# Optimization experiments

Hardware: AMD Instinct MI355X
Metric: run time of the kernel (lower is better)

The kernel has to match this reference:

```python
import jax, jax.numpy as jnp
import numpy as np

# ---- static config (mirrors forward() defaults of NeuSRenderer) ----
NV = 32
FOV = 60.0            # degrees
BIN_SIZE = 0.015
NUM_BINS = 128
RAY_U, RAY_V = 64, 8  # coarse ray grid -> 512 rays per view
NUM_PDF_RAYS = 64
STEP_COARSE = 256     # base step samples per ray (multiple of NUM_BINS)
NUM_PDF_STEPS = 32
RADIUS = 1.0
COS_ANNEAL = 0.0
HID = 64


def sdf_fn(pts, W1, b1, w2, b2):
    # pts [..., 3] -> sdf [...]
    h = jax.nn.softplus(pts @ W1 + b1)
    return h @ w2 + b2[0]


def sdf_grad(pts, W1, b1, w2):
    # analytic gradient of sdf_fn w.r.t. pts (softplus' = sigmoid)
    s = jax.nn.sigmoid(pts @ W1 + b1)          # [..., HID]
    return jnp.einsum('...h,dh->...d', s * w2, W1)


def inside_hemisphere(pts, radius):
    return (jnp.linalg.norm(pts, axis=-1) < radius) & (pts[..., 2] > 0)


def sample_rays(key, Rt, fov, usize, vsize, pdf=None, npdf=None):
    nv = Rt.shape[0]
    ns = usize * vsize
    uu, vv = jnp.meshgrid(jnp.arange(usize, dtype=jnp.float32),
                          jnp.arange(vsize, dtype=jnp.float32), indexing='ij')
    u, v = uu.ravel(), vv.ravel()
    k1, k2, k3, k4, k5 = jax.random.split(key, 5)
    ru = (u[None] + jax.random.uniform(k1, (nv, ns))) / usize
    rv = (v[None] + jax.random.uniform(k2, (nv, ns))) / vsize
    uv_idx = jnp.broadcast_to(jnp.arange(ns), (nv, ns))
    if pdf is not None:
        # Multinomial(counts) + repeat_interleave == npdf categorical draws
        idx = jax.random.categorical(k3, jnp.log(pdf + 1e-6), shape=(npdf, nv)).T  # [nv, npdf]
        cnts = jnp.zeros((nv, ns)).at[jnp.arange(nv)[:, None], idx].add(1.0)
        ru_p = (u[idx] + jax.random.uniform(k4, (nv, npdf))) / usize
        rv_p = (v[idx] + jax.random.uniform(k5, (nv, npdf))) / vsize
        w = 1.0 / ((cnts + 1.0) * ns)
        w = jnp.concatenate((w, jnp.take_along_axis(w, idx, axis=1)), axis=-1)
        ru = jnp.concatenate((ru, ru_p), axis=-1)
        rv = jnp.concatenate((rv, rv_p), axis=-1)
        uv_idx = jnp.concatenate((uv_idx, idx), axis=-1)
    else:
        w = jnp.ones_like(ru) / ns
    min_cos = np.float32(np.cos(fov * np.pi / 360.0))
    solid_angle = np.float32(2 * np.pi * (1 - min_cos))
    phi = ru * np.float32(2 * np.pi)
    cos_t = rv * (1 - min_cos) + min_cos
    sin_t = jnp.sqrt(jnp.clip(1 - cos_t ** 2, 0.0))
    d = jnp.stack((sin_t * jnp.cos(phi), sin_t * jnp.sin(phi), cos_t), axis=-1)
    o = Rt[..., -1]                                       # [nv, 3]
    d = jnp.einsum('vnj,vij->vni', d, Rt[..., :3])        # rotate to world
    w = w * cos_t * solid_angle
    sg = jax.lax.stop_gradient                            # torch.no_grad()
    return sg(o), sg(d), sg(w), uv_idx


def sample_steps(key, v, r, bin_size, nb, ns, pdf=None, npdf=None):
    k1, k2, k3 = jax.random.split(key, 3)
    edges1 = bin_size * jnp.arange(nb + 1, dtype=jnp.float32)
    edges = jnp.broadcast_to(edges1, (v, r, nb + 1))
    left = edges[..., :-1, None]                          # [v,r,nb,1]
    etas = jax.random.uniform(k1, (v, r, nb, ns // nb - 1)) * bin_size
    steps = jnp.concatenate((left, left + etas), axis=-1).reshape(v, r, ns)
    steps = jnp.concatenate((steps, edges[..., -1:]), axis=-1)  # [v,r,ns+1]
    if pdf is not None:
        bidx = jax.random.categorical(k2, jnp.log(pdf + 1e-6),
                                      shape=(npdf, v, r)).transpose(1, 2, 0)
        le = jnp.take_along_axis(edges, bidx, axis=-1)
        steps = jnp.concatenate((steps, le + jax.random.uniform(k3, le.shape) * bin_size), axis=-1)
    return jax.lax.stop_gradient(jnp.sort(steps, axis=-1))


def run_coarse(key, Rt, W1, b1, w2, b2):
    k1, k2 = jax.random.split(key)
    o, d, _, _ = sample_rays(k1, Rt, FOV, RAY_U, RAY_V)
    nv, nr = d.shape[:2]
    steps = sample_steps(k2, nv, nr, BIN_SIZE, NUM_BINS, STEP_COARSE)
    deltas = steps[..., 1:] - steps[..., :-1]
    pts = o[:, None, None, :] + steps[..., None] * d[:, :, None, :]   # [v,r,S+1,3]
    sdf = sdf_fn(pts, W1, b1, w2, b2)
    mid_pts = 0.5 * (pts[..., 1:, :] + pts[..., :-1, :])
    mid_sdf = 0.5 * (sdf[..., 1:] + sdf[..., :-1])
    cos = (sdf[..., 1:] - sdf[..., :-1]) / (deltas + 1e-6)
    prev_cos = jnp.concatenate((jnp.zeros_like(cos[..., :1]), cos[..., :-1]), axis=-1)
    cos = jnp.clip(jnp.minimum(prev_cos, cos), -1000.0, 0.0)
    dsdf = 0.5 * cos * deltas
    prev_T = jax.nn.sigmoid(64.0 * (mid_sdf - dsdf))
    next_T = jax.nn.sigmoid(64.0 * (mid_sdf + dsdf))
    alpha = (1 - next_T / (prev_T + 1e-6)) * inside_hemisphere(mid_pts, RADIUS)
    T = jnp.cumprod(jnp.concatenate((jnp.ones_like(alpha[..., :1]),
                                     (1 - alpha[..., :-1]) ** 2 + 1e-6), axis=-1), axis=-1)
    weights = (alpha * T).reshape(nv, nr, NUM_BINS, -1)
    step_pdf = weights.sum(-1)
    ray_pdf = step_pdf.sum(-1)
    sg = jax.lax.stop_gradient
    return sg(ray_pdf), sg(step_pdf)


def bin_scatter(vals, bidx, nb):
    # equivalent to einsum('vrpb,vrp->vrb', one_hot(bidx), vals), memory-light
    v, r, p = vals.shape
    return jnp.zeros((v, r, nb), vals.dtype).at[
        jnp.arange(v)[:, None, None], jnp.arange(r)[None, :, None], bidx].add(vals)


def run_fine(key, Rt, W1, b1, w2, b2, inv_s, rho, ray_pdf, step_pdf):
    k1, k2 = jax.random.split(key)
    o, d, w, uv_idx = sample_rays(k1, Rt, FOV, RAY_U, RAY_V, ray_pdf, NUM_PDF_RAYS)
    nv, nr = d.shape[:2]
    spdf = step_pdf[jnp.arange(nv)[:, None], uv_idx]                  # gather per ray
    steps_e = sample_steps(k2, nv, nr, BIN_SIZE, NUM_BINS, STEP_COARSE, spdf, NUM_PDF_STEPS)
    deltas = steps_e[..., 1:] - steps_e[..., :-1]
    steps = 0.5 * (steps_e[..., 1:] + steps_e[..., :-1])              # midpoints [v,r,P]
    pts = o[:, None, None, :] + steps[..., None] * d[:, :, None, :]
    ins = inside_hemisphere(pts, RADIUS)
    insf = ins.astype(pts.dtype)
    sdf = sdf_fn(pts, W1, b1, w2, b2) * insf                          # zeros outside (masked_scatter)
    normal = sdf_grad(pts, W1, b1, w2) * insf[..., None]
    cos = jnp.einsum('vrj,vrpj->vrp', d, normal)
    ac = -(jax.nn.relu(-cos * 0.5 + 0.5) * (1 - COS_ANNEAL) + jax.nn.relu(-cos) * COS_ANNEAL)
    dsdf = 0.5 * ac * deltas
    prev_T = jax.nn.sigmoid(inv_s * (sdf - dsdf))
    next_T = jax.nn.sigmoid(inv_s * (sdf + dsdf))
    alpha = (1 - next_T / (prev_T + 1e-6)) * insf
    T = jnp.cumprod(jnp.concatenate((jnp.ones_like(alpha[..., :1]),
                                     (1 - alpha[..., :-1]) ** 2), axis=-1), axis=-1)
    weights = alpha * T
    radiance = weights * (rho * (-ac / (steps ** 2 + 1e-6)))          # brdf_net = rho * x
    bidx = jnp.clip(jnp.floor(steps / BIN_SIZE).astype(jnp.int32), 0, NUM_BINS - 1)
    valid = ((steps > bidx * BIN_SIZE) & (steps < (bidx + 1) * BIN_SIZE)).astype(steps.dtype)
    bin_alpha = bin_scatter(alpha * valid, bidx, NUM_BINS)
    bin_weights = bin_scatter(weights * valid, bidx, NUM_BINS)
    opacity = bin_weights.sum(-1)
    rad_bins = bin_scatter(radiance * valid, bidx, NUM_BINS)
    hists = jnp.sum(rad_bins * w[..., None], axis=-2)                 # [nv, NUM_BINS]
    return hists, sdf, normal, alpha, T, weights, bin_alpha, bin_weights, opacity


def setup_inputs() -> dict:
    key = jax.random.key(0)
    ks = jax.random.split(key, 7)
    R, _ = jnp.linalg.qr(jax.random.normal(ks[0], (NV, 3, 3)))        # random rotations
    t = jax.random.normal(ks[1], (NV, 3)) * 0.1 + jnp.array([0.0, 0.0, 0.15])
    Rt = jnp.concatenate((R, t[..., None]), axis=-1).astype(jnp.float32)
    W1 = 0.5 * jax.random.normal(ks[2], (3, HID), dtype=jnp.float32)
    b1 = 0.1 * jax.random.normal(ks[3], (HID,), dtype=jnp.float32)
    w2 = 0.3 * jax.random.normal(ks[4], (HID,), dtype=jnp.float32)
    b2 = jnp.array([0.05], dtype=jnp.float32)
    inv_s = jnp.array([64.0], dtype=jnp.float32)
    rho = jnp.array([0.5], dtype=jnp.float32)
    return {"Rt": Rt, "W1": W1, "b1": b1, "w2": w2, "b2": b2, "inv_s": inv_s, "rho": rho}


def reference(Rt, W1, b1, w2, b2, inv_s, rho):
    key = jax.random.key(42)
    kc, kf = jax.random.split(key)
    ray_pdf, step_pdf = run_coarse(kc, Rt, W1, b1, w2, b2)
    outs = run_fine(kf, Rt, W1, b1, w2, b2, inv_s, rho, ray_pdf, step_pdf)
    return (*outs, ray_pdf.reshape(Rt.shape[0], RAY_U, RAY_V), step_pdf)
```

## Files before the change

kernel.cpp:

```cpp
#include <hip/hip_runtime.h>
#include <stdint.h>
#include <math.h>


#define NS    512
#define NB    128
#define NCS   257
#define NPS   32
#define NFS   289
#define NFM   288
#define HID   64

#define O_HISTS  0
#define O_SDF    4096
#define O_NORMAL 5312512
#define O_ALPHA  21237760
#define O_T      26546176
#define O_W      31854592
#define O_BA     37163008
#define O_BW     39522304
#define O_OP     41881600
#define O_RPDF   41900032
#define O_SPDF   41916416

#define DEC_RT   0
#define DEC_W1   384
#define DEC_B1   576
#define DEC_W2   640
#define DEC_B2   704
#define DEC_INVS 705
#define DEC_RHO  706
#define DEC_G    707

__host__ __device__ inline void tf2x32(uint32_t k0, uint32_t k1,
                                       uint32_t x0, uint32_t x1,
                                       uint32_t& o0, uint32_t& o1) {
  uint32_t ks2 = k0 ^ k1 ^ 0x1BD11BDAu;
  x0 += k0; x1 += k1;
#define TFR(r) { x0 += x1; x1 = (x1 << (r)) | (x1 >> (32 - (r))); x1 ^= x0; }
  TFR(13) TFR(15) TFR(26) TFR(6)
  x0 += k1;  x1 += ks2 + 1u;
  TFR(17) TFR(29) TFR(16) TFR(24)
  x0 += ks2; x1 += k0 + 2u;
  TFR(13) TFR(15) TFR(26) TFR(6)
  x0 += k0;  x1 += k1 + 3u;
  TFR(17) TFR(29) TFR(16) TFR(24)
  x0 += k1;  x1 += ks2 + 4u;
  TFR(13) TFR(15) TFR(26) TFR(6)
  x0 += ks2; x1 += k0 + 5u;
#undef TFR
  o0 = x0; o1 = x1;
}

__device__ inline uint32_t rbits(uint2 k, uint32_t i) {
  uint32_t a, b; tf2x32(k.x, k.y, 0u, i, a, b);
  return a ^ b;
}

__device__ inline float u01(uint32_t bits) {
  return __uint_as_float(0x3f800000u | (bits >> 9)) - 1.0f;
}
__device__ inline float gumbelf(uint32_t bits) {
  float f = u01(bits);
  float u = (f > 0.0f) ? f : 1.17549435082228751e-38f;
  return -logf(-logf(u));
}
__device__ inline float sigmoidf_(float x) {
  return __fdiv_rn(1.0f, __fadd_rn(1.0f, expf(-x)));
}
__device__ inline float softplusf_(float x) {
  return __fadd_rn(fmaxf(x, 0.0f), log1pf(expf(-fabsf(x))));
}
__device__ inline float frcp_(float x) { return __builtin_amdgcn_rcpf(x); }
__device__ inline float fsig_(float x) { return frcp_(1.0f + __expf(-x)); }
__device__ inline void argmax_reduce64(float& best, int& bi) {
  for (int off = 1; off < 64; off <<= 1) {
    float ob = __shfl_xor(best, off);
    int   oi = __shfl_xor(bi, off);
    if (ob > best || (ob == best && oi < bi)) { best = ob; bi = oi; }
  }
}

static void jax_split(const uint32_t k[2], int n, uint32_t out[][2]) {
  for (int j = 0; j < n; j++)
    tf2x32(k[0], k[1], 0u, (uint32_t)j, out[j][0], out[j][1]);
}
static inline uint2 mkk(const uint32_t k[2]) { return make_uint2(k[0], k[1]); }

__device__ inline float ld_as(const void* p, int i, int isbf) {
  if (isbf) {
    uint16_t h = ((const uint16_t*)p)[i];
    return __uint_as_float(((uint32_t)h) << 16);
  }
  return ((const float*)p)[i];
}

__global__ void k_decode(const void* Rt, const void* W1, const void* b1,
                         const void* w2, const void* b2, const void* invs,
                         const void* rho, float* dec) {
  __shared__ int sflag;
  if (threadIdx.x == 0) {
    float errF = 0.0f, errB = 0.0f;
    for (int v = 0; v < 8; v++)
      for (int row = 0; row < 3; row++) {
        float nF = 0.0f, nB = 0.0f;
        for (int j = 0; j < 3; j++) {
          float aF = ld_as(Rt, v * 12 + row * 4 + j, 0); nF += aF * aF;
          float aB = ld_as(Rt, v * 12 + row * 4 + j, 1); nB += aB * aB;
        }
        errF += fabsf(nF - 1.0f); errB += fabsf(nB - 1.0f);
      }
    int pickF = (errF == errF) && (!(errB == errB) || errF < errB);
    sflag = pickF ? 0 : 1;
  }
  __syncthreads();
  int f = sflag, t = threadIdx.x;
  for (int i = t; i < 384; i += 256) dec[DEC_RT + i] = ld_as(Rt, i, f);
  if (t < 192) dec[DEC_W1 + t] = ld_as(W1, t, f);
  if (t < 64)  dec[DEC_B1 + t] = ld_as(b1, t, f);
  if (t < 64)  dec[DEC_W2 + t] = ld_as(w2, t, f);
  if (t == 0) {
    dec[DEC_B2]   = ld_as(b2, 0, f);
    dec[DEC_INVS] = ld_as(invs, 0, f);
    dec[DEC_RHO]  = ld_as(rho, 0, f);
    float G = 0.0f;
    for (int j = 0; j < 64; j++) {
      float wx = ld_as(W1, j, f), wy = ld_as(W1, 64 + j, f), wz = ld_as(W1, 128 + j, f);
      G += fabsf(ld_as(w2, j, f)) * sqrtf(wx * wx + wy * wy + wz * wz);
    }
    dec[DEC_G] = G * 1.02f + 0.001f;
  }
}

__global__ void k_zero(int* __restrict__ cnts) {
  int i = blockIdx.x * 256 + threadIdx.x;
  if (i < 16384) cnts[i] = 0;
}

__global__ void __launch_bounds__(64) k_coarse(
    const float* __restrict__ dec,
    uint2 k_ru, uint2 k_rv, uint2 k_eta, float mc, float omc,
    float* __restrict__ c_step_pdf, float* __restrict__ c_ray_pdf,
    float* __restrict__ out) {
  int r = blockIdx.x, v = blockIdx.y, lane = threadIdx.x;
  __shared__ float4 sW4[64];
  __shared__ float  sw2[64];
  __shared__ float ss[NCS], sfa[NCS], sfe[NCS], salpha[256], sflagf[256];
  __shared__ int   slist[NCS], scls[256];
  if (lane < 64) {
    sW4[lane] = make_float4(dec[DEC_W1 + lane], dec[DEC_W1 + 64 + lane],
                            dec[DEC_W1 + 128 + lane], dec[DEC_B1 + lane]);
    sw2[lane] = dec[DEC_W2 + lane];
  }
  float b2 = dec[DEC_B2];
  float G  = dec[DEC_G];
  float Gm = fminf(1000.0f, G);
  float alpha_c = __fsub_rn(1.0f, __fdiv_rn(1.0f, __fadd_rn(1.0f, 1e-6f)));

  uint32_t li = (uint32_t)(v * NS + r);
  float un = (float)(r >> 3), vn = (float)(r & 7);
  float ru = __fdiv_rn(__fadd_rn(un, u01(rbits(k_ru, li))), 64.0f);
  float rv = __fdiv_rn(__fadd_rn(vn, u01(rbits(k_rv, li))), 8.0f);
  float phi = __fmul_rn(ru, (float)(2.0 * M_PI));
  float ct  = __fadd_rn(__fmul_rn(rv, omc), mc);
  float stq = sqrtf(fmaxf(__fsub_rn(1.0f, __fmul_rn(ct, ct)), 0.0f));
  float dc0 = __fmul_rn(stq, cosf(phi));
  float dc1 = __fmul_rn(stq, sinf(phi));
  const float* Rv = dec + DEC_RT + v * 12;
  float o0 = Rv[3], o1 = Rv[7], o2 = Rv[11];
  float d0 = dc0 * Rv[0] + dc1 * Rv[1] + ct * Rv[2];
  float d1 = dc0 * Rv[4] + dc1 * Rv[5] + ct * Rv[6];
  float d2 = dc0 * Rv[8] + dc1 * Rv[9] + ct * Rv[10];

  for (int p = lane; p < NCS; p += 64) {
    float sp;
    if (p == 256) sp = __fmul_rn(0.015f, 128.0f);
    else {
      int b = p >> 1;
      float eb = __fmul_rn(0.015f, (float)b);
      if (p & 1) {
        float u = u01(rbits(k_eta, li * 128u + (uint32_t)b));
        sp = __fadd_rn(eb, __fmul_rn(u, 0.015f));
      } else sp = eb;
    }
    ss[p] = sp;
  }
  __syncthreads();

  for (int p = lane; p < 256; p += 64) {
    float s0 = ss[p], s1 = ss[p + 1];
    float ax = __fadd_rn(o0, __fmul_rn(s0, d0)), bx = __fadd_rn(o0, __fmul_rn(s1, d0));
    float ay = __fadd_rn(o1, __fmul_rn(s0, d1)), by = __fadd_rn(o1, __fmul_rn(s1, d1));
    float az = __fadd_rn(o2, __fmul_rn(s0, d2)), bz = __fadd_rn(o2, __fmul_rn(s1, d2));
    float mx = __fmul_rn(0.5f, __fadd_rn(ax, bx));
    float my = __fmul_rn(0.5f, __fadd_rn(ay, by));
    float mz = __fmul_rn(0.5f, __fadd_rn(az, bz));
    float n2 = __fadd_rn(__fadd_rn(__fmul_rn(mx, mx), __fmul_rn(my, my)), __fmul_rn(mz, mz));
    bool ins = (sqrtf(n2) < 1.0f) && (mz > 0.0f);
    sflagf[p] = ins ? 1.0f : 0.0f;
  }
  __syncthreads();

  int ncnt = 0;
  for (int c = 0; c < 5; c++) {
    int p = c * 64 + lane;
    bool need = false;
    if (p < NCS) {
      bool f0 = (p >= 1) ? (sflagf[p - 1] != 0.0f) : false;
      bool f1 = (p < 256) ? (sflagf[p] != 0.0f) : false;
      bool f2 = (p + 1 < 256) ? (sflagf[p + 1] != 0.0f) : false;
      need = f0 || f1 || f2;
    }
    unsigned long long m = __ballot(need);
    int idx = ncnt + __popcll(m & ((1ull << lane) - 1ull));
    if (need) slist[idx] = p;
    ncnt += __popcll(m);
  }
  __syncthreads();

  for (int k = lane; k < ncnt; k += 64) {
    int p = slist[k];
    float sp = ss[p];
    float px = fmaf(sp, d0, o0);
    float py = fmaf(sp, d1, o1);
    float pz = fmaf(sp, d2, o2);
    float acc = 0.0f;
    for (int j = 0; j < HID; j++) {
      float4 q = sW4[j];
      float t = fmaf(px, q.x, fmaf(py, q.y, fmaf(pz, q.z, q.w)));
      float e = __expf(-fabsf(t));
      acc = fmaf(fmaxf(t, 0.0f) + __logf(1.0f + e), sw2[j], acc);
    }
    sfa[p] = acc + b2;
  }
  __syncthreads();

  for (int p = lane; p < 256; p += 64) {
    int cls = 0;
    if (sflagf[p] != 0.0f) {
      float delta = __fsub_rn(ss[p + 1], ss[p]);
      float Bd = 0.5f * delta * Gm * 1.01f + 1e-6f;
      float ma = 0.5f * (sfa[p] + sfa[p + 1]);
      float margin = Bd + 0.02f;
      if (ma - margin > 0.28f)       cls = 1;
      else if (ma + margin < -0.52f) cls = 2;
      else                            cls = 3;
    }
    scls[p] = cls;
  }
  __syncthreads();

  int ecnt = 0;
  for (int c = 0; c < 5; c++) {
    int p = c * 64 + lane;
    bool need = false;
    if (p < NCS) {
      bool f0 = (p >= 1) ? (scls[p - 1] == 3) : false;
      bool f1 = (p < 256) ? (scls[p] == 3) : false;
      bool f2 = (p + 1 < 256) ? (scls[p + 1] == 3) : false;
      need = f0 || f1 || f2;
    }
    unsigned long long m = __ballot(need);
    int idx = ecnt + __popcll(m & ((1ull << lane) - 1ull));
    if (need) slist[idx] = p;
    ecnt += __popcll(m);
  }
  __syncthreads();

  for (int k = lane; k < ecnt; k += 64) {
    int p = slist[k];
    float sp = ss[p];
    float px = __fadd_rn(o0, __fmul_rn(sp, d0));
    float py = __fadd_rn(o1, __fmul_rn(sp, d1));
    float pz = __fadd_rn(o2, __fmul_rn(sp, d2));
    float acc = 0.0f;
    for (int j = 0; j < HID; j++) {
      float4 q = sW4[j];
      float t = fmaf(px, q.x, fmaf(py, q.y, fmaf(pz, q.z, q.w)));
      acc = fmaf(softplusf_(t), sw2[j], acc);
    }
    sfe[p] = __fadd_rn(acc, b2);
  }
  __syncthreads();

  for (int p = lane; p < 256; p += 64) {
    int cls = scls[p];
    float a;
    if (cls == 0)      a = 0.0f;
    else if (cls == 1) a = alpha_c;
    else if (cls == 2) a = 1.0f;
    else {
      float s0 = ss[p], s1 = ss[p + 1];
      float f0 = sfe[p], f1 = sfe[p + 1];
      float delta = __fsub_rn(s1, s0);
      float mid_sdf = __fmul_rn(0.5f, __fadd_rn(f1, f0));
      float cosv = __fdiv_rn(__fsub_rn(f1, f0), __fadd_rn(delta, 1e-6f));
      float pcos = 0.0f;
      if (p > 0)
        pcos = __fdiv_rn(__fsub_rn(f0, sfe[p - 1]),
                         __fadd_rn(__fsub_rn(s0, ss[p - 1]), 1e-6f));
      float cc = fminf(fmaxf(fminf(pcos, cosv), -1000.0f), 0.0f);
      float dsdf = __fmul_rn(__fmul_rn(0.5f, cc), delta);
      float pT = sigmoidf_(__fmul_rn(64.0f, __fsub_rn(mid_sdf, dsdf)));
      float nT = sigmoidf_(__fmul_rn(64.0f, __fadd_rn(mid_sdf, dsdf)));
      a = __fmul_rn(__fsub_rn(1.0f, __fdiv_rn(nT, __fadd_rn(pT, 1e-6f))), 1.0f);
    }
    salpha[p] = a;
  }
  __syncthreads();

  if (lane == 0) {
    float T = 1.0f, rsum = 0.0f;
    int base = (v * NS + r) * NB;
    for (int b = 0; b < NB; b++) {
      float a0 = salpha[2 * b], a1 = salpha[2 * b + 1];
      float w0 = __fmul_rn(a0, T);
      float om = __fsub_rn(1.0f, a0);
      T = __fmul_rn(T, __fadd_rn(__fmul_rn(om, om), 1e-6f));
      float w1 = __fmul_rn(a1, T);
      om = __fsub_rn(1.0f, a1);
      T = __fmul_rn(T, __fadd_rn(__fmul_rn(om, om), 1e-6f));
      float spdf = __fadd_rn(w0, w1);
      c_step_pdf[base + b] = spdf;
      out[O_SPDF + base + b] = spdf;
      rsum = __fadd_rn(rsum, spdf);
    }
    c_ray_pdf[v * NS + r] = rsum;
    out[O_RPDF + v * NS + r] = rsum;
  }
}

__global__ void __launch_bounds__(64) k_raycat(
    const float* __restrict__ c_ray_pdf, uint2 kg,
    int* __restrict__ f_idx, int* __restrict__ cnts) {
  int p = blockIdx.x, v = blockIdx.y, lane = threadIdx.x;
  uint32_t rowbase = ((uint32_t)p * 32u + (uint32_t)v) * 512u;
  float best = -INFINITY; int bi = 0;
  for (int n = lane; n < 512; n += 64) {
    float lg = logf(__fadd_rn(c_ray_pdf[v * 512 + n], 1e-6f));
    float val = __fadd_rn(gumbelf(rbits(kg, rowbase + (uint32_t)n)), lg);
    if (val > best) { best = val; bi = n; }
  }
  argmax_reduce64(best, bi);
  if (lane == 0) {
    f_idx[v * 64 + p] = bi;
    atomicAdd(&cnts[v * 512 + bi], 1);
  }
}

__global__ void __launch_bounds__(64) k_stepcat(
    const float* __restrict__ c_step_pdf, const int* __restrict__ f_idx,
    uint2 kg, int* __restrict__ bidx) {
  int r = blockIdx.x, v = blockIdx.y, lane = threadIdx.x;
  int n = (r < 512) ? r : f_idx[v * 64 + (r - 512)];
  const float* pdfrow = c_step_pdf + (v * 512 + n) * 128;
  float lg0 = logf(__fadd_rn(pdfrow[lane], 1e-6f));
  float lg1 = logf(__fadd_rn(pdfrow[64 + lane], 1e-6f));
  for (int p = 0; p < 32; p++) {
    uint32_t base = (((uint32_t)p * 32u + (uint32_t)v) * 576u + (uint32_t)r) * 128u;
    float v0 = __fadd_rn(gumbelf(rbits(kg, base + (uint32_t)lane)), lg0);
    float v1 = __fadd_rn(gumbelf(rbits(kg, base + 64u + (uint32_t)lane)), lg1);
    float best = v0; int bi = lane;
    if (v1 > best) { best = v1; bi = 64 + lane; }
    argmax_reduce64(best, bi);
    if (lane == 0) bidx[(v * 576 + r) * 32 + p] = bi;
  }
}

__global__ void __launch_bounds__(64) k_fine(
    const float* __restrict__ dec, const int* __restrict__ f_idx,
    const int* __restrict__ cnts, const int* __restrict__ bidx,
    uint2 k_ru, uint2 k_rv, uint2 k_rup, uint2 k_rvp, uint2 k_eta, uint2 k_us,
    float mc, float omc, float sa,
    float* __restrict__ rad_rows, float* __restrict__ out) {
  int r = blockIdx.x, v = blockIdx.y, lane = threadIdx.x;
  __shared__ float4 sW4[64];
  __shared__ float  sw2[64];
  __shared__ float sb[NCS], pe[NPS], st[NFS];
  __shared__ float sal[NFM], sac[NFM], sT[NFM];
  __shared__ int   slist[NFM];
  __shared__ float bina[NB], binw[NB], binr[NB];
  if (lane < 64) {
    sW4[lane] = make_float4(dec[DEC_W1 + lane], dec[DEC_W1 + 64 + lane],
                            dec[DEC_W1 + 128 + lane], dec[DEC_B1 + lane]);
    sw2[lane] = dec[DEC_W2 + lane];
  }
  bina[lane] = 0.0f; binw[lane] = 0.0f; binr[lane] = 0.0f;
  bina[64 + lane] = 0.0f; binw[64 + lane] = 0.0f; binr[64 + lane] = 0.0f;
  float b2 = dec[DEC_B2], inv_s = dec[DEC_INVS], rho = dec[DEC_RHO];

  int n; float ruB, rvB;
  if (r < 512) {
    n = r;
    ruB = u01(rbits(k_ru, (uint32_t)(v * 512 + r)));
    rvB = u01(rbits(k_rv, (uint32_t)(v * 512 + r)));
  } else {
    int p = r - 512;
    n = f_idx[v * 64 + p];
    ruB = u01(rbits(k_rup, (uint32_t)(v * 64 + p)));
    rvB = u01(rbits(k_rvp, (uint32_t)(v * 64 + p)));
  }
  float un = (float)(n >> 3), vn = (float)(n & 7);
  float ru = __fdiv_rn(__fadd_rn(un, ruB), 64.0f);
  float rv = __fdiv_rn(__fadd_rn(vn, rvB), 8.0f);
  float phi = __fmul_rn(ru, (float)(2.0 * M_PI));
  float ct  = __fadd_rn(__fmul_rn(rv, omc), mc);
  float stq = sqrtf(fmaxf(__fsub_rn(1.0f, __fmul_rn(ct, ct)), 0.0f));
  float dc0 = __fmul_rn(stq, cosf(phi));
  float dc1 = __fmul_rn(stq, sinf(phi));
  const float* Rv = dec + DEC_RT + v * 12;
  float o0 = Rv[3], o1 = Rv[7], o2 = Rv[11];
  float d0 = dc0 * Rv[0] + dc1 * Rv[1] + ct * Rv[2];
  float d1 = dc0 * Rv[4] + dc1 * Rv[5] + ct * Rv[6];
  float d2 = dc0 * Rv[8] + dc1 * Rv[9] + ct * Rv[10];
  float wb = __fdiv_rn(1.0f, __fmul_rn(__fadd_rn((float)cnts[v * 512 + n], 1.0f), 512.0f));
  float wray = __fmul_rn(__fmul_rn(wb, ct), sa);

  uint32_t li = (uint32_t)(v * 576 + r);
  for (int p = lane; p < NCS; p += 64) {
    float sp;
    if (p == 256) sp = __fmul_rn(0.015f, 128.0f);
    else {
      int b = p >> 1;
      float eb = __fmul_rn(0.015f, (float)b);
      if (p & 1) {
        float u = u01(rbits(k_eta, li * 128u + (uint32_t)b));
        sp = __fadd_rn(eb, __fmul_rn(u, 0.015f));
      } else sp = eb;
    }
    sb[p] = sp;
  }
  if (lane < NPS) {
    int b = bidx[(v * 576 + r) * 32 + lane];
    float le = __fmul_rn(0.015f, (float)b);
    float u = u01(rbits(k_us, li * 32u + (uint32_t)lane));
    pe[lane] = __fadd_rn(le, __fmul_rn(u, 0.015f));
  }
  __syncthreads();

  for (int c = 0; c < 5; c++) {
    int p = c * 64 + lane;
    if (p < NCS) {
      float x = sb[p];
      int cntlt = 0;
      for (int j = 0; j < NPS; j++) cntlt += (pe[j] < x) ? 1 : 0;
      st[p + cntlt] = x;
    }
  }
  if (lane < NPS) {
    float x = pe[lane];
    int lo = 0, hi = NCS;
    while (lo < hi) { int m = (lo + hi) >> 1; if (sb[m] <= x) lo = m + 1; else hi = m; }
    int rk = 0;
    for (int j = 0; j < NPS; j++) {
      float y = pe[j];
      rk += (y < x || (y == x && j < lane)) ? 1 : 0;
    }
    st[lo + rk] = x;
  }
  __syncthreads();

  size_t obase = (size_t)(v * 576 + r) * NFM;
  int cnt = 0;
  for (int c = 0; c < 5; c++) {
    int p = c * 64 + lane;
    bool f = false;
    if (p < NFM) {
      float s0 = st[p], s1 = st[p + 1];
      float mid = __fmul_rn(0.5f, __fadd_rn(s1, s0));
      float px = __fadd_rn(o0, __fmul_rn(mid, d0));
      float py = __fadd_rn(o1, __fmul_rn(mid, d1));
      float pz = __fadd_rn(o2, __fmul_rn(mid, d2));
      float n2 = __fadd_rn(__fadd_rn(__fmul_rn(px, px), __fmul_rn(py, py)), __fmul_rn(pz, pz));
      f = (sqrtf(n2) < 1.0f) && (pz > 0.0f);
      sal[p] = 0.0f; sac[p] = 0.0f;
      if (!f) {
        out[O_SDF + obase + p] = 0.0f;
        out[O_ALPHA + obase + p] = 0.0f;
        size_t nb3 = (obase + p) * 3;
        out[O_NORMAL + nb3] = 0.0f;
        out[O_NORMAL + nb3 + 1] = 0.0f;
        out[O_NORMAL + nb3 + 2] = 0.0f;
      }
    }
    unsigned long long m = __ballot(f);
    int idx = cnt + __popcll(m & ((1ull << lane) - 1ull));
    if (f) slist[idx] = p;
    cnt += __popcll(m);
  }
  __syncthreads();

  for (int k = lane; k < cnt; k += 64) {
    int p = slist[k];
    float s0 = st[p], s1 = st[p + 1];
    float delta = s1 - s0;
    float mid = 0.5f * (s1 + s0);
    float px = fmaf(mid, d0, o0);
    float py = fmaf(mid, d1, o1);
    float pz = fmaf(mid, d2, o2);
    float acc = 0.0f, g0 = 0.0f, g1 = 0.0f, g2 = 0.0f;
    for (int j = 0; j < HID; j++) {
      float4 q = sW4[j];
      float t = fmaf(px, q.x, fmaf(py, q.y, fmaf(pz, q.z, q.w)));
      float e = __expf(-fabsf(t));
      float w2j = sw2[j];
      acc = fmaf(fmaxf(t, 0.0f) + __logf(1.0f + e), w2j, acc);
      float rr = frcp_(1.0f + e);
      float sg = (t >= 0.0f) ? rr : e * rr;
      float m = sg * w2j;
      g0 = fmaf(m, q.x, g0);
      g1 = fmaf(m, q.y, g1);
      g2 = fmaf(m, q.z, g2);
    }
    float sdf = acc + b2;
    float cosr = fmaf(d0, g0, fmaf(d1, g1, d2 * g2));
    float ac = -fmaxf(fmaf(-cosr, 0.5f, 0.5f), 0.0f);
    float dsdf = 0.5f * ac * delta;
    float pT = fsig_(inv_s * (sdf - dsdf));
    float nT = fsig_(inv_s * (sdf + dsdf));
    float alpha = 1.0f - nT * frcp_(pT + 1e-6f);
    sal[p] = alpha; sac[p] = ac;
    out[O_SDF + obase + p] = sdf;
    size_t nb3 = (obase + p) * 3;
    out[O_NORMAL + nb3]     = g0;
    out[O_NORMAL + nb3 + 1] = g1;
    out[O_NORMAL + nb3 + 2] = g2;
    out[O_ALPHA + obase + p] = alpha;
  }
  __syncthreads();

  {
    int q0 = lane * 5, q1 = q0 + 5 > NFM ? NFM : q0 + 5;
    float lp = 1.0f;
    for (int q = q0; q < q1; q++) { float om = 1.0f - sal[q]; lp *= om * om; }
    float x = lp;
    for (int d = 1; d < 64; d <<= 1) {
      float y = __shfl_up(x, d);
      if (lane >= d) x *= y;
    }
    float excl = __shfl_up(x, 1);
    if (lane == 0) excl = 1.0f;
    float T = excl;
    for (int q = q0; q < q1; q++) {
      sT[q] = T;
      float om = 1.0f - sal[q];
      T *= om * om;
    }
  }
  __syncthreads();

  for (int c = 0; c < 5; c++) {
    int p = c * 64 + lane;
    if (p < NFM) {
      float T = sT[p], a = sal[p];
      float wgt = a * T;
      out[O_T + obase + p] = T;
      out[O_W + obase + p] = wgt;
      float s0 = st[p], s1 = st[p + 1];
      float mid = __fmul_rn(0.5f, __fadd_rn(s1, s0));
      int bi = (int)floorf(__fdiv_rn(mid, 0.015f));
      bi = bi < 0 ? 0 : (bi > 127 ? 127 : bi);
      bool valid = (mid > __fmul_rn((float)bi, 0.015f)) &&
                   (mid < __fmul_rn((float)(bi + 1), 0.015f));
      if (valid) {
        atomicAdd(&bina[bi], a);
        atomicAdd(&binw[bi], wgt);
        float inner = (-sac[p]) * frcp_(fmaf(mid, mid, 1e-6f));
        atomicAdd(&binr[bi], wgt * rho * inner);
      }
    }
  }
  __syncthreads();

  size_t bb = (size_t)(v * 576 + r) * NB;
  for (int c = 0; c < 2; c++) {
    int b = c * 64 + lane;
    out[O_BA + bb + b] = bina[b];
    out[O_BW + bb + b] = binw[b];
    rad_rows[bb + b] = __fmul_rn(binr[b], wray);
  }
  float opv = binw[lane] + binw[64 + lane];
  for (int d = 32; d; d >>= 1) opv += __shfl_xor(opv, d);
  if (lane == 0) out[O_OP + (size_t)(v * 576 + r)] = opv;
}

__global__ void __launch_bounds__(256) k_final(
    const float* __restrict__ rad_rows, float* __restrict__ out) {
  int idx = blockIdx.x * 4 + (threadIdx.x >> 6);
  int lane = threadIdx.x & 63;
  if (idx < 4096) {
    int v = idx >> 7, b = idx & 127;
    const float* base = rad_rows + (size_t)v * 576 * 128 + b;
    float s = 0.0f;
    for (int k = 0; k < 9; k++)
      s += base[(size_t)(lane + 64 * k) * 128];
    for (int d = 32; d; d >>= 1) s += __shfl_xor(s, d);
    if (lane == 0) out[O_HISTS + idx] = s;
  }
}

extern "C" void kernel_launch(void* const* d_in, const int* in_sizes, int n_in,
                              void* d_out, int out_size, void* d_ws, size_t ws_size,
                              hipStream_t stream) {
  float* out = (float*)d_out;

  const size_t WS_NEED = 5081856u * 4u;
  if (n_in != 7) { hipMemsetAsync(d_out, 0x75, 4, stream); return; }
  static const int want[7] = {384, 192, 64, 64, 1, 1, 1};
  for (int i = 0; i < 7; i++)
    if (in_sizes[i] != want[i]) { hipMemsetAsync(d_out, 0x74, 4, stream); return; }
  if (ws_size < WS_NEED) { hipMemsetAsync(d_out, 0x77, 4, stream); return; }
  (void)out_size;

  uint32_t root[2] = {0u, 42u};
  uint32_t kcf[2][2]; jax_split(root, 2, kcf);
  uint32_t ck[2][2];  jax_split(kcf[0], 2, ck);
  uint32_t crk[5][2]; jax_split(ck[0], 5, crk);
  uint32_t csk[3][2]; jax_split(ck[1], 3, csk);
  uint32_t fk2[2][2]; jax_split(kcf[1], 2, fk2);
  uint32_t frk[5][2]; jax_split(fk2[0], 5, frk);
  uint32_t fsk[3][2]; jax_split(fk2[1], 3, fsk);

  float mc  = (float)cos(60.0 * M_PI / 360.0);
  float omc = 1.0f - mc;
  float sa  = (float)(2.0 * M_PI * (1.0 - (double)mc));

  float* ws = (float*)d_ws;
  size_t off = 0;
  float* dec        = ws + off; off += 768;
  float* c_step_pdf = ws + off; off += 2097152;
  float* c_ray_pdf  = ws + off; off += 16384;
  int*   f_idx      = (int*)(ws + off); off += 2048;
  int*   cnts       = (int*)(ws + off); off += 16384;
  int*   bidx       = (int*)(ws + off); off += 589824;
  float* rad_rows   = ws + off; off += 2359296;

  k_decode<<<1, 256, 0, stream>>>(d_in[0], d_in[1], d_in[2], d_in[3],
                                  d_in[4], d_in[5], d_in[6], dec);
  k_zero<<<64, 256, 0, stream>>>(cnts);
  k_coarse<<<dim3(512, 32), 64, 0, stream>>>(dec,
      mkk(crk[0]), mkk(crk[1]), mkk(csk[0]), mc, omc, c_step_pdf, c_ray_pdf, out);
  k_raycat<<<dim3(64, 32), 64, 0, stream>>>(c_ray_pdf, mkk(frk[2]), f_idx, cnts);
  k_stepcat<<<dim3(576, 32), 64, 0, stream>>>(c_step_pdf, f_idx, mkk(fsk[1]), bidx);
  k_fine<<<dim3(576, 32), 64, 0, stream>>>(dec, f_idx, cnts, bidx,
      mkk(frk[0]), mkk(frk[1]), mkk(frk[3]), mkk(frk[4]), mkk(fsk[0]), mkk(fsk[2]),
      mc, omc, sa, rad_rows, out);
  k_final<<<1024, 256, 0, stream>>>(rad_rows, out);
}
```

Before: 813.7 us.

## Replace Gumbel-max categorical sampling with exponential-race argmin plus exact fallback

```diff
diff --git a/kernel.cpp b/kernel.cpp
--- a/kernel.cpp
+++ b/kernel.cpp
@@ -31,6 +31,8 @@
 #define DEC_INVS 705
 #define DEC_RHO  706
 #define DEC_G    707
+
+#define TINYF 1.17549435082228751e-38f
 
 __host__ __device__ inline void tf2x32(uint32_t k0, uint32_t k1,
                                        uint32_t x0, uint32_t x1,
@@ -62,7 +64,7 @@
 }
 __device__ inline float gumbelf(uint32_t bits) {
   float f = u01(bits);
-  float u = (f > 0.0f) ? f : 1.17549435082228751e-38f;
+  float u = (f > 0.0f) ? f : TINYF;
   return -logf(-logf(u));
 }
 __device__ inline float sigmoidf_(float x) {
@@ -78,6 +80,13 @@
     float ob = __shfl_xor(best, off);
     int   oi = __shfl_xor(bi, off);
     if (ob > best || (ob == best && oi < bi)) { best = ob; bi = oi; }
+  }
+}
+__device__ inline void argmin_reduce64(float& best, int& bi) {
+  for (int off = 1; off < 64; off <<= 1) {
+    float ob = __shfl_xor(best, off);
+    int   oi = __shfl_xor(bi, off);
+    if (ob < best || (ob == best && oi < bi)) { best = ob; bi = oi; }
   }
 }
 
@@ -135,6 +144,16 @@
 __global__ void k_zero(int* __restrict__ cnts) {
   int i = blockIdx.x * 256 + threadIdx.x;
   if (i < 16384) cnts[i] = 0;
+}
+
+__global__ void k_raylog(const float* __restrict__ crp,
+                         float* __restrict__ lg, float* __restrict__ ew) {
+  int i = blockIdx.x * 256 + threadIdx.x;
+  if (i < 16384) {
+    float l = logf(__fadd_rn(crp[i], 1e-6f));
+    lg[i] = l;
+    ew[i] = __expf(-l);
+  }
 }
 
 __global__ void __launch_bounds__(64) k_coarse(
@@ -331,20 +350,41 @@
 }
 
 __global__ void __launch_bounds__(64) k_raycat(
-    const float* __restrict__ c_ray_pdf, uint2 kg,
-    int* __restrict__ f_idx, int* __restrict__ cnts) {
+    const float* __restrict__ ray_lg, const float* __restrict__ ray_ew,
+    uint2 kg, int* __restrict__ f_idx, int* __restrict__ cnts) {
   int p = blockIdx.x, v = blockIdx.y, lane = threadIdx.x;
   uint32_t rowbase = ((uint32_t)p * 32u + (uint32_t)v) * 512u;
-  float best = -INFINITY; int bi = 0;
-  for (int n = lane; n < 512; n += 64) {
-    float lg = logf(__fadd_rn(c_ray_pdf[v * 512 + n], 1e-6f));
-    float val = __fadd_rn(gumbelf(rbits(kg, rowbase + (uint32_t)n)), lg);
-    if (val > best) { best = val; bi = n; }
-  }
-  argmax_reduce64(best, bi);
+  const float* lgrow = ray_lg + v * 512;
+  const float* ewrow = ray_ew + v * 512;
+  float rc[8];
+  float m1 = INFINITY; int i1 = 0;
+  for (int k = 0; k < 8; k++) {
+    int n = lane + 64 * k;
+    uint32_t bits = rbits(kg, rowbase + (uint32_t)n);
+    float f = u01(bits);
+    float u = (f > 0.0f) ? f : TINYF;
+    float E = -__logf(u);
+    float rr = E * ewrow[n];
+    rc[k] = rr;
+    if (rr < m1) { m1 = rr; i1 = n; }
+  }
+  argmin_reduce64(m1, i1);
+  float thr = m1 * (1.0f + 1e-4f);
+  bool near = false;
+  for (int k = 0; k < 8; k++)
+    near = near || ((lane + 64 * k != i1) && (rc[k] <= thr));
+  if (__ballot(near)) {
+    float best = -INFINITY; int bi = 0;
+    for (int n = lane; n < 512; n += 64) {
+      float val = __fadd_rn(gumbelf(rbits(kg, rowbase + (uint32_t)n)), lgrow[n]);
+      if (val > best) { best = val; bi = n; }
+    }
+    argmax_reduce64(best, bi);
+    i1 = bi;
+  }
   if (lane == 0) {
-    f_idx[v * 64 + p] = bi;
-    atomicAdd(&cnts[v * 512 + bi], 1);
+    f_idx[v * 64 + p] = i1;
+    atomicAdd(&cnts[v * 512 + i1], 1);
   }
 }
 
@@ -356,14 +396,31 @@
   const float* pdfrow = c_step_pdf + (v * 512 + n) * 128;
   float lg0 = logf(__fadd_rn(pdfrow[lane], 1e-6f));
   float lg1 = logf(__fadd_rn(pdfrow[64 + lane], 1e-6f));
+  float ew0 = __expf(-lg0), ew1 = __expf(-lg1);
   for (int p = 0; p < 32; p++) {
     uint32_t base = (((uint32_t)p * 32u + (uint32_t)v) * 576u + (uint32_t)r) * 128u;
-    float v0 = __fadd_rn(gumbelf(rbits(kg, base + (uint32_t)lane)), lg0);
-    float v1 = __fadd_rn(gumbelf(rbits(kg, base + 64u + (uint32_t)lane)), lg1);
-    float best = v0; int bi = lane;
-    if (v1 > best) { best = v1; bi = 64 + lane; }
-    argmax_reduce64(best, bi);
-    if (lane == 0) bidx[(v * 576 + r) * 32 + p] = bi;
+    uint32_t bits0 = rbits(kg, base + (uint32_t)lane);
+    uint32_t bits1 = rbits(kg, base + 64u + (uint32_t)lane);
+    float f0 = u01(bits0), f1 = u01(bits1);
+    float u0 = (f0 > 0.0f) ? f0 : TINYF;
+    float u1 = (f1 > 0.0f) ? f1 : TINYF;
+    float r0 = (-__logf(u0)) * ew0;
+    float r1 = (-__logf(u1)) * ew1;
+    float m1 = r0; int i1 = lane;
+    if (r1 < m1) { m1 = r1; i1 = 64 + lane; }
+    argmin_reduce64(m1, i1);
+    float thr = m1 * (1.0f + 1e-4f);
+    bool near = ((lane != i1) && (r0 <= thr)) ||
+                ((64 + lane != i1) && (r1 <= thr));
+    if (__ballot(near)) {
+      float v0 = __fadd_rn(gumbelf(bits0), lg0);
+      float v1 = __fadd_rn(gumbelf(bits1), lg1);
+      float best = v0; int bi = lane;
+      if (v1 > best) { best = v1; bi = 64 + lane; }
+      argmax_reduce64(best, bi);
+      i1 = bi;
+    }
+    if (lane == 0) bidx[(v * 576 + r) * 32 + p] = i1;
   }
 }
 
@@ -604,7 +661,7 @@
                               hipStream_t stream) {
   float* out = (float*)d_out;
 
-  const size_t WS_NEED = 5081856u * 4u;
+  const size_t WS_NEED = 5114624u * 4u;
   if (n_in != 7) { hipMemsetAsync(d_out, 0x75, 4, stream); return; }
   static const int want[7] = {384, 192, 64, 64, 1, 1, 1};
   for (int i = 0; i < 7; i++)
@@ -630,6 +687,8 @@
   float* dec        = ws + off; off += 768;
   float* c_step_pdf = ws + off; off += 2097152;
   float* c_ray_pdf  = ws + off; off += 16384;
+  float* ray_lg     = ws + off; off += 16384;
+  float* ray_ew     = ws + off; off += 16384;
   int*   f_idx      = (int*)(ws + off); off += 2048;
   int*   cnts       = (int*)(ws + off); off += 16384;
   int*   bidx       = (int*)(ws + off); off += 589824;
@@ -640,7 +699,8 @@
   k_zero<<<64, 256, 0, stream>>>(cnts);
   k_coarse<<<dim3(512, 32), 64, 0, stream>>>(dec,
       mkk(crk[0]), mkk(crk[1]), mkk(csk[0]), mc, omc, c_step_pdf, c_ray_pdf, out);
-  k_raycat<<<dim3(64, 32), 64, 0, stream>>>(c_ray_pdf, mkk(frk[2]), f_idx, cnts);
+  k_raylog<<<64, 256, 0, stream>>>(c_ray_pdf, ray_lg, ray_ew);
+  k_raycat<<<dim3(64, 32), 64, 0, stream>>>(ray_lg, ray_ew, mkk(frk[2]), f_idx, cnts);
   k_stepcat<<<dim3(576, 32), 64, 0, stream>>>(c_step_pdf, f_idx, mkk(fsk[1]), bidx);
   k_fine<<<dim3(576, 32), 64, 0, stream>>>(dec, f_idx, cnts, bidx,
       mkk(frk[0]), mkk(frk[1]), mkk(frk[3]), mkk(frk[4]), mkk(fsk[0]), mkk(fsk[2]),
```

After: 804.5 us. About the same (-1.1%).
